# Kernel optimization log

Measured on AMD Instinct MI355X. Metric: run time of the kernel, lower is better.

The kernel has to match this reference:

```python
import jax, jax.numpy as jnp
import numpy as np

L, D, H, F, V, S, B = 6, 1024, 16, 4096, 32000, 1024, 2
HD = D // H  # head_dim = 64


def _rope_tables():
    freqs = 1.0 / (10000.0 ** (np.arange(0, HD, 2, dtype=np.float32) / HD))
    ang = np.outer(np.arange(S, dtype=np.float32), freqs)
    ang = np.concatenate([ang, ang], axis=-1)  # angles.repeat(1, 2)
    return jnp.asarray(np.cos(ang)), jnp.asarray(np.sin(ang))


def _ln(x, g, b):
    m = jnp.mean(x, -1, keepdims=True)
    v = jnp.mean((x - m) ** 2, -1, keepdims=True)
    return (x - m) * jax.lax.rsqrt(v + 1e-5) * g + b


def _rot_half(x):
    h = x.shape[-1] // 2
    return jnp.concatenate([-x[..., h:], x[..., :h]], -1)


def _gate(sig, W1, b1, W2, b2):
    h = jax.nn.gelu(sig @ W1 + b1, approximate=False)
    return jax.nn.sigmoid(h @ W2 + b2)[:, None, :]  # (B,1,D)


def setup_inputs():
    key = jax.random.key(0)
    ks = iter(jax.random.split(key, 40))

    def nrm(shape, s=0.02):
        return jax.random.normal(next(ks), shape, jnp.float32) * s

    cos, sin = _rope_tables()
    return {
        "input_ids": jax.random.randint(next(ks), (B, S), 0, V, dtype=jnp.int32),
        "gate_signals": jax.random.uniform(next(ks), (B, 3), jnp.float32),
        "tok_emb": nrm((V, D)),
        "rope_cos": cos, "rope_sin": sin,
        "Wq": nrm((L, D, D)), "bq": jnp.zeros((L, D)),
        "Wk": nrm((L, D, D)), "bk": jnp.zeros((L, D)),
        "Wv": nrm((L, D, D)), "bv": jnp.zeros((L, D)),
        "Wo": nrm((L, D, D)), "bo": jnp.zeros((L, D)),
        "ln1_g": jnp.ones((L, D)), "ln1_b": jnp.zeros((L, D)),
        "ln2_g": jnp.ones((L, D)), "ln2_b": jnp.zeros((L, D)),
        "W1": nrm((L, D, F)), "b1": jnp.zeros((L, F)),
        "W2": nrm((L, F, D)), "b2": jnp.zeros((L, D)),
        "ag_W1": nrm((L, 3, 32)), "ag_b1": jnp.zeros((L, 32)),
        "ag_W2": nrm((L, 32, D)), "ag_b2": jnp.full((L, D), 2.0, jnp.float32),
        "fg_W1": nrm((L, 3, 32)), "fg_b1": jnp.zeros((L, 32)),
        "fg_W2": nrm((L, 32, D)), "fg_b2": jnp.full((L, D), 2.0, jnp.float32),
        "lnf_g": jnp.ones((D,)), "lnf_b": jnp.zeros((D,)),
        "Wout": nrm((D, V)), "bout": jnp.zeros((V,)),
    }


def _forward(input_ids, gate_signals, tok_emb, rope_cos, rope_sin,
             Wq, bq, Wk, bk, Wv, bv, Wo, bo,
             ln1_g, ln1_b, ln2_g, ln2_b, W1, b1, W2, b2,
             ag_W1, ag_b1, ag_W2, ag_b2, fg_W1, fg_b1, fg_W2, fg_b2,
             lnf_g, lnf_b, Wout, bout):
    x = tok_emb[input_ids]  # (B,S,D)
    cos = rope_cos[None, :, None, :]  # broadcast over batch, heads
    sin = rope_sin[None, :, None, :]
    causal = jnp.triu(jnp.ones((S, S), bool), 1)
    scale = 1.0 / np.sqrt(HD).astype(np.float32)
    for i in range(L):
        n = _ln(x, ln1_g[i], ln1_b[i])
        q = (n @ Wq[i] + bq[i]).reshape(B, S, H, HD)
        k = (n @ Wk[i] + bk[i]).reshape(B, S, H, HD)
        v = (n @ Wv[i] + bv[i]).reshape(B, S, H, HD)
        q = q * cos + _rot_half(q) * sin
        k = k * cos + _rot_half(k) * sin
        scores = jnp.einsum("bqhd,bkhd->bhqk", q, k) * scale
        scores = jnp.where(causal[None, None], -jnp.inf, scores)
        attn = jax.nn.softmax(scores, axis=-1)
        ao = jnp.einsum("bhqk,bkhd->bqhd", attn, v).reshape(B, S, D)
        ao = (ao @ Wo[i] + bo[i]) * _gate(gate_signals, ag_W1[i], ag_b1[i], ag_W2[i], ag_b2[i])
        x = x + ao
        n = _ln(x, ln2_g[i], ln2_b[i])
        f = jax.nn.gelu(n @ W1[i] + b1[i], approximate=False) @ W2[i] + b2[i]
        f = f * _gate(gate_signals, fg_W1[i], fg_b1[i], fg_W2[i], fg_b2[i])
        x = x + f
    x = _ln(x, lnf_g, lnf_b)
    return x @ Wout + bout  # logits (B,S,V)


def reference(input_ids, gate_signals, tok_emb, rope_cos, rope_sin,
              Wq, bq, Wk, bk, Wv, bv, Wo, bo,
              ln1_g, ln1_b, ln2_g, ln2_b, W1, b1, W2, b2,
              ag_W1, ag_b1, ag_W2, ag_b2, fg_W1, fg_b1, fg_W2, fg_b2,
              lnf_g, lnf_b, Wout, bout):
    return _forward(input_ids, gate_signals, tok_emb, rope_cos, rope_sin,
                    Wq, bq, Wk, bk, Wv, bv, Wo, bo,
                    ln1_g, ln1_b, ln2_g, ln2_b, W1, b1, W2, b2,
                    ag_W1, ag_b1, ag_W2, ag_b2, fg_W1, fg_b1, fg_W2, fg_b2,
                    lnf_g, lnf_b, Wout, bout)
```

## Files before the change

kernel.cpp:

```cpp
#include <hip/hip_runtime.h>


typedef __attribute__((ext_vector_type(8))) short short8;
typedef __attribute__((ext_vector_type(4))) float f32x4;

__device__ inline unsigned short f2bf(float f) {
  unsigned u = __builtin_bit_cast(unsigned, f);
  u += 0x7fffu + ((u >> 16) & 1u);
  return (unsigned short)(u >> 16);
}

__device__ inline void gload_lds16(const unsigned short* g, unsigned short* l) {
  __builtin_amdgcn_global_load_lds(
      (const __attribute__((address_space(1))) void*)g,
      (__attribute__((address_space(3))) void*)l, 16, 0, 0);
}

__global__ __launch_bounds__(256) void transpose_k(
    const float* __restrict__ src, unsigned short* __restrict__ dst,
    int K, int N, size_t srcStride, size_t dstStride) {
  __shared__ __align__(16) float tile[32 * 33];
  src += (size_t)blockIdx.z * srcStride;
  dst += (size_t)blockIdx.z * dstStride;
  const int k0 = blockIdx.y * 32, n0 = blockIdx.x * 32;
  const int t = threadIdx.x;
  {
    int k = t >> 3, n4 = (t & 7) << 2;
    float4 v = *(const float4*)&src[(size_t)(k0 + k) * N + n0 + n4];
    tile[k * 33 + n4 + 0] = v.x; tile[k * 33 + n4 + 1] = v.y;
    tile[k * 33 + n4 + 2] = v.z; tile[k * 33 + n4 + 3] = v.w;
  }
  __syncthreads();
  {
    int n = t >> 3, k4 = (t & 7) << 2;
    ushort4 o;
    o.x = f2bf(tile[(k4 + 0) * 33 + n]);
    o.y = f2bf(tile[(k4 + 1) * 33 + n]);
    o.z = f2bf(tile[(k4 + 2) * 33 + n]);
    o.w = f2bf(tile[(k4 + 3) * 33 + n]);
    *(ushort4*)&dst[(size_t)(n0 + n) * K + k0 + k4] = o;
  }
}

__global__ __launch_bounds__(256) void embed_k(
    const int* __restrict__ ids, const float* __restrict__ emb,
    float* __restrict__ x) {
  const int m = blockIdx.x, t = threadIdx.x;
  const int id = ids[m];
  ((float4*)(x + (size_t)m * 1024))[t] = ((const float4*)(emb + (size_t)id * 1024))[t];
}

__global__ __launch_bounds__(256) void gates_k(
    const float* __restrict__ sig,
    const float* __restrict__ aW1, const float* __restrict__ ab1,
    const float* __restrict__ aW2, const float* __restrict__ ab2,
    const float* __restrict__ fW1, const float* __restrict__ fb1,
    const float* __restrict__ fW2, const float* __restrict__ fb2,
    float* __restrict__ gout) {
  const int b = blockIdx.x, l = blockIdx.y, w = blockIdx.z;
  const float* W1 = (w ? fW1 : aW1) + l * 96;
  const float* B1 = (w ? fb1 : ab1) + l * 32;
  const float* W2 = (w ? fW2 : aW2) + (size_t)l * 32 * 1024;
  const float* B2 = (w ? fb2 : ab2) + l * 1024;
  __shared__ float h[32];
  const int t = threadIdx.x;
  if (t < 32) {
    float a = sig[b * 3] * W1[t] + sig[b * 3 + 1] * W1[32 + t] + sig[b * 3 + 2] * W1[64 + t] + B1[t];
    h[t] = 0.5f * a * (1.0f + erff(a * 0.70710678118654752f));
  }
  __syncthreads();
  #pragma unroll
  for (int i = 0; i < 4; i++) {
    int d = t + i * 256;
    float a = B2[d];
    #pragma unroll
    for (int j = 0; j < 32; j++) a += h[j] * W2[j * 1024 + d];
    gout[(((size_t)w * 6 + l) * 2 + b) * 1024 + d] = 1.0f / (1.0f + expf(-a));
  }
}

__global__ __launch_bounds__(256) void ln_k(
    const float* __restrict__ x, const float* __restrict__ gw,
    const float* __restrict__ bw, unsigned short* __restrict__ out) {
  const int row = blockIdx.x, t = threadIdx.x;
  const float4 v = ((const float4*)(x + (size_t)row * 1024))[t];
  float s  = v.x + v.y + v.z + v.w;
  float s2 = v.x * v.x + v.y * v.y + v.z * v.z + v.w * v.w;
  #pragma unroll
  for (int m_ = 1; m_ < 64; m_ <<= 1) {
    s  += __shfl_xor(s, m_, 64);
    s2 += __shfl_xor(s2, m_, 64);
  }
  __shared__ float red[8];
  const int wv = t >> 6;
  if ((t & 63) == 0) { red[wv] = s; red[4 + wv] = s2; }
  __syncthreads();
  s  = red[0] + red[1] + red[2] + red[3];
  s2 = red[4] + red[5] + red[6] + red[7];
  const float mean = s * (1.0f / 1024.0f);
  const float var  = s2 * (1.0f / 1024.0f) - mean * mean;
  const float rstd = rsqrtf(var + 1e-5f);
  const float4 gv = ((const float4*)gw)[t];
  const float4 bv = ((const float4*)bw)[t];
  ushort4 o;
  o.x = f2bf((v.x - mean) * rstd * gv.x + bv.x);
  o.y = f2bf((v.y - mean) * rstd * gv.y + bv.y);
  o.z = f2bf((v.z - mean) * rstd * gv.z + bv.z);
  o.w = f2bf((v.w - mean) * rstd * gv.w + bv.w);
  ((ushort4*)(out + (size_t)row * 1024))[t] = o;
}

struct GArgs {
  const unsigned short *A, *Bt0, *Bt1, *Bt2;
  const float *bias0, *bias1, *bias2;
  unsigned short *ob0, *ob1, *ob2;
  float* xio;
  const float *gate, *ropec, *ropes;
  int M, N, K, epi;
};

template <int MT>
__global__ __launch_bounds__(256) void gemm_bt(GArgs g) {
  constexpr int BM = MT * 32;
  __shared__ __align__(16) unsigned short As[BM * 64];
  __shared__ __align__(16) unsigned short Bs[128 * 64];
  const int z = blockIdx.z;
  const unsigned short* A  = g.A;
  const unsigned short* Bt = (z == 0) ? g.Bt0 : (z == 1 ? g.Bt1 : g.Bt2);
  unsigned short* obf      = (z == 0) ? g.ob0 : (z == 1 ? g.ob1 : g.ob2);
  const float* bias        = (z == 0) ? g.bias0 : (z == 1 ? g.bias1 : g.bias2);
  const int m0 = blockIdx.y * BM, n0 = blockIdx.x * 128;
  const int t = threadIdx.x;
  const int wave = t >> 6, lane = t & 63, l16 = lane & 15, quad = lane >> 4;
  const int wm = wave >> 1, wn = wave & 1;
  const int K_ = g.K;

  const int srow = lane >> 3;
  const int scol = (lane & 7) ^ srow;

  const f32x4 vzero = {0.0f, 0.0f, 0.0f, 0.0f};
  f32x4 acc[MT][4];
  #pragma unroll
  for (int i = 0; i < MT; i++)
    #pragma unroll
    for (int j = 0; j < 4; j++) acc[i][j] = vzero;

  for (int k0 = 0; k0 < K_; k0 += 64) {
    __syncthreads();
    #pragma unroll
    for (int i = 0; i < MT; i++) {
      const int r0 = (wave * MT + i) * 8;
      gload_lds16(&A[(size_t)(m0 + r0 + srow) * K_ + k0 + scol * 8], &As[r0 * 64]);
    }
    #pragma unroll
    for (int i = 0; i < 4; i++) {
      const int r0 = (wave * 4 + i) * 8;
      gload_lds16(&Bt[(size_t)(n0 + r0 + srow) * K_ + k0 + scol * 8], &Bs[r0 * 64]);
    }
    __syncthreads();
    #pragma unroll
    for (int kk = 0; kk < 2; kk++) {
      short8 af[MT], bfr[4];
      #pragma unroll
      for (int mt = 0; mt < MT; mt++) {
        const int ar = wm * (MT * 16) + mt * 16 + l16;
        af[mt] = *(const short8*)&As[ar * 64 + (((kk * 4 + quad) ^ (ar & 7)) << 3)];
      }
      #pragma unroll
      for (int nt = 0; nt < 4; nt++) {
        const int br = wn * 64 + nt * 16 + l16;
        bfr[nt] = *(const short8*)&Bs[br * 64 + (((kk * 4 + quad) ^ (br & 7)) << 3)];
      }
      #pragma unroll
      for (int mt = 0; mt < MT; mt++)
        #pragma unroll
        for (int nt = 0; nt < 4; nt++)
          acc[mt][nt] = __builtin_amdgcn_mfma_f32_16x16x32_bf16(af[mt], bfr[nt], acc[mt][nt], 0, 0, 0);
    }
  }

  const int mbase = m0 + wm * (MT * 16) + quad * 4;
  const int nb = n0 + wn * 64 + l16;
  const size_t Nsz = (size_t)g.N;
  float bv4[4];
  #pragma unroll
  for (int nt = 0; nt < 4; nt++) bv4[nt] = bias[nb + nt * 16];

  if (g.epi == 1 && z < 2) {
    #pragma unroll
    for (int mt = 0; mt < MT; mt++) {
      float vv[4][4];
      #pragma unroll
      for (int nt = 0; nt < 4; nt++)
        #pragma unroll
        for (int r = 0; r < 4; r++) vv[nt][r] = acc[mt][nt][r] + bv4[nt];
      #pragma unroll
      for (int nt = 0; nt < 4; nt++) {
        const int d = (nb + nt * 16) & 63;
        #pragma unroll
        for (int r = 0; r < 4; r++) {
          const int m = mbase + mt * 16 + r;
          const int s = m & 1023;
          const float c = g.ropec[s * 64 + d], sn = g.ropes[s * 64 + d];
          const float rot = (nt < 2) ? -vv[nt + 2][r] : vv[nt - 2][r];
          obf[(size_t)m * Nsz + nb + nt * 16] = f2bf(vv[nt][r] * c + rot * sn);
        }
      }
    }
  } else if (g.epi <= 1) {
    #pragma unroll
    for (int mt = 0; mt < MT; mt++)
      #pragma unroll
      for (int nt = 0; nt < 4; nt++)
        #pragma unroll
        for (int r = 0; r < 4; r++)
          obf[(size_t)(mbase + mt * 16 + r) * Nsz + nb + nt * 16] = f2bf(acc[mt][nt][r] + bv4[nt]);
  } else if (g.epi == 2) {
    const int bb = m0 >> 10;
    float gt[4];
    #pragma unroll
    for (int nt = 0; nt < 4; nt++) gt[nt] = g.gate[bb * 1024 + nb + nt * 16];
    #pragma unroll
    for (int mt = 0; mt < MT; mt++)
      #pragma unroll
      for (int nt = 0; nt < 4; nt++)
        #pragma unroll
        for (int r = 0; r < 4; r++) {
          const size_t idx = (size_t)(mbase + mt * 16 + r) * Nsz + nb + nt * 16;
          g.xio[idx] += (acc[mt][nt][r] + bv4[nt]) * gt[nt];
        }
  } else if (g.epi == 3) {
    #pragma unroll
    for (int mt = 0; mt < MT; mt++)
      #pragma unroll
      for (int nt = 0; nt < 4; nt++)
        #pragma unroll
        for (int r = 0; r < 4; r++) {
          float vg = acc[mt][nt][r] + bv4[nt];
          vg = 0.5f * vg * (1.0f + erff(vg * 0.70710678118654752f));
          obf[(size_t)(mbase + mt * 16 + r) * Nsz + nb + nt * 16] = f2bf(vg);
        }
  } else {
    #pragma unroll
    for (int mt = 0; mt < MT; mt++)
      #pragma unroll
      for (int nt = 0; nt < 4; nt++)
        #pragma unroll
        for (int r = 0; r < 4; r++)
          g.xio[(size_t)(mbase + mt * 16 + r) * Nsz + nb + nt * 16] = acc[mt][nt][r] + bv4[nt];
  }
}

__global__ __launch_bounds__(64) void attn_k(
    const unsigned short* __restrict__ q, const unsigned short* __restrict__ k,
    const unsigned short* __restrict__ v, unsigned short* __restrict__ o) {
  __shared__ __align__(16) unsigned short Pl[32 * 72];
  __shared__ __align__(16) unsigned short Vt[64 * 72];
  const int lane = threadIdx.x, l16 = lane & 15, quad = lane >> 4;
  const int bh = blockIdx.y, b = bh >> 4, h = bh & 15;
  const int q0 = blockIdx.x * 32;
  const size_t base = (size_t)b * 1024 * 1024 + h * 64;
  const unsigned short* qh = q + base;
  const unsigned short* kh = k + base;
  const unsigned short* vh = v + base;
  unsigned short* oh = o + base;

  const f32x4 vzero = {0.0f, 0.0f, 0.0f, 0.0f};
  short8 qf[2][2];
  #pragma unroll
  for (int mt = 0; mt < 2; mt++)
    #pragma unroll
    for (int kt = 0; kt < 2; kt++)
      qf[mt][kt] = *(const short8*)&qh[(size_t)(q0 + mt * 16 + l16) * 1024 + kt * 32 + quad * 8];

  f32x4 oacc[2][4];
  float mrun[2][4], lrun[2][4];
  #pragma unroll
  for (int mt = 0; mt < 2; mt++) {
    #pragma unroll
    for (int jt = 0; jt < 4; jt++) oacc[mt][jt] = vzero;
    #pragma unroll
    for (int r = 0; r < 4; r++) { mrun[mt][r] = -1e30f; lrun[mt][r] = 0.0f; }
  }

  const int tmax = (q0 + 31) >> 6;
  for (int tt = 0; tt <= tmax; tt++) {
    const int s0 = tt * 64;
    short8 kf[4][2];
    #pragma unroll
    for (int st = 0; st < 4; st++)
      #pragma unroll
      for (int kt = 0; kt < 2; kt++)
        kf[st][kt] = *(const short8*)&kh[(size_t)(s0 + st * 16 + l16) * 1024 + kt * 32 + quad * 8];

    __syncthreads();
    {
      const int p = lane & 31, c0 = lane >> 5;
      #pragma unroll
      for (int i = 0; i < 4; i++) {
        const int d0 = (c0 + i * 2) * 8;
        uint4 va = *(const uint4*)&vh[(size_t)(s0 + 2 * p) * 1024 + d0];
        uint4 vb = *(const uint4*)&vh[(size_t)(s0 + 2 * p + 1) * 1024 + d0];
        const unsigned short* pa = (const unsigned short*)&va;
        const unsigned short* pb = (const unsigned short*)&vb;
        #pragma unroll
        for (int j = 0; j < 8; j++)
          *(unsigned*)&Vt[(d0 + j) * 72 + 2 * p] =
              (unsigned)pa[j] | ((unsigned)pb[j] << 16);
      }
    }

    f32x4 sacc[2][4];
    #pragma unroll
    for (int mt = 0; mt < 2; mt++)
      #pragma unroll
      for (int st = 0; st < 4; st++) sacc[mt][st] = vzero;
    #pragma unroll
    for (int mt = 0; mt < 2; mt++)
      #pragma unroll
      for (int st = 0; st < 4; st++)
        #pragma unroll
        for (int kt = 0; kt < 2; kt++)
          sacc[mt][st] = __builtin_amdgcn_mfma_f32_16x16x32_bf16(qf[mt][kt], kf[st][kt], sacc[mt][st], 0, 0, 0);

    float sv[2][4][4];
    #pragma unroll
    for (int mt = 0; mt < 2; mt++)
      #pragma unroll
      for (int st = 0; st < 4; st++)
        #pragma unroll
        for (int r = 0; r < 4; r++) {
          float x = sacc[mt][st][r] * 0.125f;
          if (tt == tmax) {
            const int qi = q0 + mt * 16 + quad * 4 + r;
            const int si = s0 + st * 16 + l16;
            if (si > qi) x = -1e30f;
          }
          sv[mt][st][r] = x;
        }

    float alpha[2][4];
    #pragma unroll
    for (int mt = 0; mt < 2; mt++)
      #pragma unroll
      for (int r = 0; r < 4; r++) {
        float rm = fmaxf(fmaxf(sv[mt][0][r], sv[mt][1][r]), fmaxf(sv[mt][2][r], sv[mt][3][r]));
        rm = fmaxf(rm, __shfl_xor(rm, 1, 64));
        rm = fmaxf(rm, __shfl_xor(rm, 2, 64));
        rm = fmaxf(rm, __shfl_xor(rm, 4, 64));
        rm = fmaxf(rm, __shfl_xor(rm, 8, 64));
        const float mn = fmaxf(mrun[mt][r], rm);
        alpha[mt][r] = __expf(mrun[mt][r] - mn);
        mrun[mt][r] = mn;
      }

    float psum[2][4] = {};
    #pragma unroll
    for (int mt = 0; mt < 2; mt++)
      #pragma unroll
      for (int st = 0; st < 4; st++)
        #pragma unroll
        for (int r = 0; r < 4; r++) {
          const float p_ = __expf(sv[mt][st][r] - mrun[mt][r]);
          psum[mt][r] += p_;
          Pl[(mt * 16 + quad * 4 + r) * 72 + st * 16 + l16] = f2bf(p_);
        }
    #pragma unroll
    for (int mt = 0; mt < 2; mt++)
      #pragma unroll
      for (int r = 0; r < 4; r++) {
        float ps = psum[mt][r];
        ps += __shfl_xor(ps, 1, 64);
        ps += __shfl_xor(ps, 2, 64);
        ps += __shfl_xor(ps, 4, 64);
        ps += __shfl_xor(ps, 8, 64);
        lrun[mt][r] = lrun[mt][r] * alpha[mt][r] + ps;
      }
    #pragma unroll
    for (int mt = 0; mt < 2; mt++)
      #pragma unroll
      for (int jt = 0; jt < 4; jt++)
        #pragma unroll
        for (int r = 0; r < 4; r++) oacc[mt][jt][r] *= alpha[mt][r];

    __syncthreads();
    short8 pf[2][2], vf[4][2];
    #pragma unroll
    for (int mt = 0; mt < 2; mt++)
      #pragma unroll
      for (int kt = 0; kt < 2; kt++)
        pf[mt][kt] = *(const short8*)&Pl[(mt * 16 + l16) * 72 + kt * 32 + quad * 8];
    #pragma unroll
    for (int jt = 0; jt < 4; jt++)
      #pragma unroll
      for (int kt = 0; kt < 2; kt++)
        vf[jt][kt] = *(const short8*)&Vt[(jt * 16 + l16) * 72 + kt * 32 + quad * 8];
    #pragma unroll
    for (int mt = 0; mt < 2; mt++)
      #pragma unroll
      for (int jt = 0; jt < 4; jt++)
        #pragma unroll
        for (int kt = 0; kt < 2; kt++)
          oacc[mt][jt] = __builtin_amdgcn_mfma_f32_16x16x32_bf16(pf[mt][kt], vf[jt][kt], oacc[mt][jt], 0, 0, 0);
  }

  #pragma unroll
  for (int mt = 0; mt < 2; mt++)
    #pragma unroll
    for (int r = 0; r < 4; r++) {
      const float inv = 1.0f / lrun[mt][r];
      const int qrow = q0 + mt * 16 + quad * 4 + r;
      #pragma unroll
      for (int jt = 0; jt < 4; jt++)
        oh[(size_t)qrow * 1024 + jt * 16 + l16] = f2bf(oacc[mt][jt][r] * inv);
    }
}

extern "C" void kernel_launch(void* const* d_in, const int* in_sizes, int n_in,
                              void* d_out, int out_size, void* d_ws, size_t ws_size,
                              hipStream_t stream) {
  const int*   ids   = (const int*)d_in[0];
  const float* sig   = (const float*)d_in[1];
  const float* temb  = (const float*)d_in[2];
  const float* ropec = (const float*)d_in[3];
  const float* ropes = (const float*)d_in[4];
  const float* Wq = (const float*)d_in[5],  *bq = (const float*)d_in[6];
  const float* Wk = (const float*)d_in[7],  *bk = (const float*)d_in[8];
  const float* Wv = (const float*)d_in[9],  *bv = (const float*)d_in[10];
  const float* Wo = (const float*)d_in[11], *bo = (const float*)d_in[12];
  const float* ln1g = (const float*)d_in[13], *ln1b = (const float*)d_in[14];
  const float* ln2g = (const float*)d_in[15], *ln2b = (const float*)d_in[16];
  const float* W1 = (const float*)d_in[17], *b1 = (const float*)d_in[18];
  const float* W2 = (const float*)d_in[19], *b2 = (const float*)d_in[20];
  const float* agW1 = (const float*)d_in[21], *agb1 = (const float*)d_in[22];
  const float* agW2 = (const float*)d_in[23], *agb2 = (const float*)d_in[24];
  const float* fgW1 = (const float*)d_in[25], *fgb1 = (const float*)d_in[26];
  const float* fgW2 = (const float*)d_in[27], *fgb2 = (const float*)d_in[28];
  const float* lnfg = (const float*)d_in[29], *lnfb = (const float*)d_in[30];
  const float* Wout = (const float*)d_in[31], *bout = (const float*)d_in[32];

  const size_t DD = 1024 * 1024;
  uintptr_t w = (uintptr_t)d_ws;
  auto take = [&](size_t bytes) -> uintptr_t {
    uintptr_t p = w; w += (bytes + 255) & ~(size_t)255; return p;
  };
  unsigned short* wt_qkv = (unsigned short*)take((size_t)6 * 3 * DD * 2);
  unsigned short* wt_o   = (unsigned short*)take((size_t)6 * DD * 2);
  unsigned short* wt_1   = (unsigned short*)take((size_t)6 * 4096 * 1024 * 2);
  unsigned short* wt_2   = (unsigned short*)take((size_t)6 * 1024 * 4096 * 2);
  unsigned short* wt_out = (unsigned short*)take((size_t)32000 * 1024 * 2);
  float*          xbuf   = (float*)take((size_t)2048 * 1024 * 4);
  unsigned short* nbuf   = (unsigned short*)take((size_t)2048 * 1024 * 2);
  unsigned short* qbuf   = (unsigned short*)take((size_t)3 * 2048 * 1024 * 2);
  unsigned short* kbuf   = qbuf + (size_t)2048 * 1024;
  unsigned short* vbuf   = kbuf + (size_t)2048 * 1024;
  unsigned short* aobuf  = (unsigned short*)take((size_t)2048 * 1024 * 2);
  unsigned short* hbuf   = (unsigned short*)take((size_t)2048 * 4096 * 2);
  float*          gbuf   = (float*)take((size_t)2 * 6 * 2 * 1024 * 4);

  transpose_k<<<dim3(32, 32, 6),  256, 0, stream>>>(Wq, wt_qkv + 0 * DD, 1024, 1024, DD, 3 * DD);
  transpose_k<<<dim3(32, 32, 6),  256, 0, stream>>>(Wk, wt_qkv + 1 * DD, 1024, 1024, DD, 3 * DD);
  transpose_k<<<dim3(32, 32, 6),  256, 0, stream>>>(Wv, wt_qkv + 2 * DD, 1024, 1024, DD, 3 * DD);
  transpose_k<<<dim3(32, 32, 6),  256, 0, stream>>>(Wo, wt_o, 1024, 1024, DD, DD);
  transpose_k<<<dim3(128, 32, 6), 256, 0, stream>>>(W1, wt_1, 1024, 4096, (size_t)4096 * 1024, (size_t)4096 * 1024);
  transpose_k<<<dim3(32, 128, 6), 256, 0, stream>>>(W2, wt_2, 4096, 1024, (size_t)4096 * 1024, (size_t)4096 * 1024);
  transpose_k<<<dim3(1000, 32, 1), 256, 0, stream>>>(Wout, wt_out, 1024, 32000, 0, 0);

  gates_k<<<dim3(2, 6, 2), 256, 0, stream>>>(sig, agW1, agb1, agW2, agb2, fgW1, fgb1, fgW2, fgb2, gbuf);
  embed_k<<<dim3(2048), 256, 0, stream>>>(ids, temb, xbuf);

  for (int l = 0; l < 6; l++) {
    ln_k<<<2048, 256, 0, stream>>>(xbuf, ln1g + l * 1024, ln1b + l * 1024, nbuf);

    GArgs a{};
    a.A = nbuf;
    a.Bt0 = wt_qkv + (size_t)(l * 3 + 0) * DD;
    a.Bt1 = wt_qkv + (size_t)(l * 3 + 1) * DD;
    a.Bt2 = wt_qkv + (size_t)(l * 3 + 2) * DD;
    a.bias0 = bq + l * 1024; a.bias1 = bk + l * 1024; a.bias2 = bv + l * 1024;
    a.ob0 = qbuf; a.ob1 = kbuf; a.ob2 = vbuf;
    a.ropec = ropec; a.ropes = ropes;
    a.M = 2048; a.N = 1024; a.K = 1024; a.epi = 1;
    gemm_bt<4><<<dim3(8, 16, 3), 256, 0, stream>>>(a);

    attn_k<<<dim3(32, 32), 64, 0, stream>>>(qbuf, kbuf, vbuf, aobuf);

    GArgs c{};
    c.A = aobuf; c.Bt0 = wt_o + (size_t)l * DD; c.bias0 = bo + l * 1024;
    c.xio = xbuf; c.gate = gbuf + (size_t)l * 2 * 1024;
    c.M = 2048; c.N = 1024; c.K = 1024; c.epi = 2;
    gemm_bt<2><<<dim3(8, 32, 1), 256, 0, stream>>>(c);

    ln_k<<<2048, 256, 0, stream>>>(xbuf, ln2g + l * 1024, ln2b + l * 1024, nbuf);

    GArgs f1{};
    f1.A = nbuf; f1.Bt0 = wt_1 + (size_t)l * 4096 * 1024; f1.bias0 = b1 + l * 4096;
    f1.ob0 = hbuf; f1.M = 2048; f1.N = 4096; f1.K = 1024; f1.epi = 3;
    gemm_bt<4><<<dim3(32, 16, 1), 256, 0, stream>>>(f1);

    GArgs f2{};
    f2.A = hbuf; f2.Bt0 = wt_2 + (size_t)l * 1024 * 4096; f2.bias0 = b2 + l * 1024;
    f2.xio = xbuf; f2.gate = gbuf + (size_t)(6 + l) * 2 * 1024;
    f2.M = 2048; f2.N = 1024; f2.K = 4096; f2.epi = 2;
    gemm_bt<2><<<dim3(8, 32, 1), 256, 0, stream>>>(f2);
  }

  ln_k<<<2048, 256, 0, stream>>>(xbuf, lnfg, lnfb, nbuf);

  GArgs lo{};
  lo.A = nbuf; lo.Bt0 = wt_out; lo.bias0 = bout;
  lo.xio = (float*)d_out;
  lo.M = 2048; lo.N = 32000; lo.K = 1024; lo.epi = 5;
  gemm_bt<4><<<dim3(250, 16, 1), 256, 0, stream>>>(lo);
}
```

Baseline: 2.235 ms.

## Remap GEMM blocks across XCDs and split attention across two waves

Measured after the change: 2.259 ms. Within noise of the previous version (+1.1%).

```diff
diff --git a/kernel.cpp b/kernel.cpp
--- a/kernel.cpp
+++ b/kernel.cpp
@@ -129,7 +129,17 @@
   const unsigned short* Bt = (z == 0) ? g.Bt0 : (z == 1 ? g.Bt1 : g.Bt2);
   unsigned short* obf      = (z == 0) ? g.ob0 : (z == 1 ? g.ob1 : g.ob2);
   const float* bias        = (z == 0) ? g.bias0 : (z == 1 ? g.bias1 : g.bias2);
-  const int m0 = blockIdx.y * BM, n0 = blockIdx.x * 128;
+
+  const int nwg  = gridDim.x * gridDim.y;
+  const int hwid = blockIdx.y * gridDim.x + blockIdx.x;
+  const int xcd = hwid & 7, j8 = hwid >> 3;
+  const int q8 = nwg >> 3, r8 = nwg & 7;
+  const int logical =
+      (xcd < r8 ? xcd * (q8 + 1) : r8 * (q8 + 1) + (xcd - r8) * q8) + j8;
+  const int mIdx = logical % gridDim.y;
+  const int nIdx = logical / gridDim.y;
+  const int m0 = mIdx * BM, n0 = nIdx * 128;
+
   const int t = threadIdx.x;
   const int wave = t >> 6, lane = t & 63, l16 = lane & 15, quad = lane >> 4;
   const int wm = wave >> 1, wn = wave & 1;
@@ -251,37 +261,35 @@
   }
 }
 
-__global__ __launch_bounds__(64) void attn_k(
+__global__ __launch_bounds__(128) void attn_k(
     const unsigned short* __restrict__ q, const unsigned short* __restrict__ k,
     const unsigned short* __restrict__ v, unsigned short* __restrict__ o) {
-  __shared__ __align__(16) unsigned short Pl[32 * 72];
+  __shared__ __align__(16) unsigned short Pl[2 * 16 * 72];
   __shared__ __align__(16) unsigned short Vt[64 * 72];
-  const int lane = threadIdx.x, l16 = lane & 15, quad = lane >> 4;
+  const int t = threadIdx.x;
+  const int wave = t >> 6, lane = t & 63, l16 = lane & 15, quad = lane >> 4;
   const int bh = blockIdx.y, b = bh >> 4, h = bh & 15;
   const int q0 = blockIdx.x * 32;
+  const int qw = q0 + wave * 16;
   const size_t base = (size_t)b * 1024 * 1024 + h * 64;
   const unsigned short* qh = q + base;
   const unsigned short* kh = k + base;
   const unsigned short* vh = v + base;
   unsigned short* oh = o + base;
+  unsigned short* Pw = Pl + wave * 16 * 72;
 
   const f32x4 vzero = {0.0f, 0.0f, 0.0f, 0.0f};
-  short8 qf[2][2];
-  #pragma unroll
-  for (int mt = 0; mt < 2; mt++)
-    #pragma unroll
-    for (int kt = 0; kt < 2; kt++)
-      qf[mt][kt] = *(const short8*)&qh[(size_t)(q0 + mt * 16 + l16) * 1024 + kt * 32 + quad * 8];
-
-  f32x4 oacc[2][4];
-  float mrun[2][4], lrun[2][4];
-  #pragma unroll
-  for (int mt = 0; mt < 2; mt++) {
-    #pragma unroll
-    for (int jt = 0; jt < 4; jt++) oacc[mt][jt] = vzero;
-    #pragma unroll
-    for (int r = 0; r < 4; r++) { mrun[mt][r] = -1e30f; lrun[mt][r] = 0.0f; }
-  }
+  short8 qf[2];
+  #pragma unroll
+  for (int kt = 0; kt < 2; kt++)
+    qf[kt] = *(const short8*)&qh[(size_t)(qw + l16) * 1024 + kt * 32 + quad * 8];
+
+  f32x4 oacc[4];
+  float mrun[4], lrun[4];
+  #pragma unroll
+  for (int jt = 0; jt < 4; jt++) oacc[jt] = vzero;
+  #pragma unroll
+  for (int r = 0; r < 4; r++) { mrun[r] = -1e30f; lrun[r] = 0.0f; }
 
   const int tmax = (q0 + 31) >> 6;
   for (int tt = 0; tt <= tmax; tt++) {
@@ -295,125 +303,105 @@
 
     __syncthreads();
     {
-      const int p = lane & 31, c0 = lane >> 5;
-      #pragma unroll
-      for (int i = 0; i < 4; i++) {
-        const int d0 = (c0 + i * 2) * 8;
+      const int p = t & 31, c0 = t >> 5;
+      #pragma unroll
+      for (int i = 0; i < 2; i++) {
+        const int d0 = (c0 + i * 4) * 8;
         uint4 va = *(const uint4*)&vh[(size_t)(s0 + 2 * p) * 1024 + d0];
         uint4 vb = *(const uint4*)&vh[(size_t)(s0 + 2 * p + 1) * 1024 + d0];
         const unsigned short* pa = (const unsigned short*)&va;
         const unsigned short* pb = (const unsigned short*)&vb;
         #pragma unroll
-        for (int j = 0; j < 8; j++)
-          *(unsigned*)&Vt[(d0 + j) * 72 + 2 * p] =
-              (unsigned)pa[j] | ((unsigned)pb[j] << 16);
+        for (int jj = 0; jj < 8; jj++)
+          *(unsigned*)&Vt[(d0 + jj) * 72 + 2 * p] =
+              (unsigned)pa[jj] | ((unsigned)pb[jj] << 16);
       }
     }
 
-    f32x4 sacc[2][4];
-    #pragma unroll
-    for (int mt = 0; mt < 2; mt++)
-      #pragma unroll
-      for (int st = 0; st < 4; st++) sacc[mt][st] = vzero;
-    #pragma unroll
-    for (int mt = 0; mt < 2; mt++)
-      #pragma unroll
-      for (int st = 0; st < 4; st++)
-        #pragma unroll
-        for (int kt = 0; kt < 2; kt++)
-          sacc[mt][st] = __builtin_amdgcn_mfma_f32_16x16x32_bf16(qf[mt][kt], kf[st][kt], sacc[mt][st], 0, 0, 0);
-
-    float sv[2][4][4];
-    #pragma unroll
-    for (int mt = 0; mt < 2; mt++)
-      #pragma unroll
-      for (int st = 0; st < 4; st++)
-        #pragma unroll
-        for (int r = 0; r < 4; r++) {
-          float x = sacc[mt][st][r] * 0.125f;
-          if (tt == tmax) {
-            const int qi = q0 + mt * 16 + quad * 4 + r;
-            const int si = s0 + st * 16 + l16;
-            if (si > qi) x = -1e30f;
-          }
-          sv[mt][st][r] = x;
+    f32x4 sacc[4];
+    #pragma unroll
+    for (int st = 0; st < 4; st++) sacc[st] = vzero;
+    #pragma unroll
+    for (int st = 0; st < 4; st++)
+      #pragma unroll
+      for (int kt = 0; kt < 2; kt++)
+        sacc[st] = __builtin_amdgcn_mfma_f32_16x16x32_bf16(qf[kt], kf[st][kt], sacc[st], 0, 0, 0);
+
+    float sv[4][4];
+    #pragma unroll
+    for (int st = 0; st < 4; st++)
+      #pragma unroll
+      for (int r = 0; r < 4; r++) {
+        float x = sacc[st][r] * 0.125f;
+        if (tt == tmax) {
+          const int qi = qw + quad * 4 + r;
+          const int si = s0 + st * 16 + l16;
+          if (si > qi) x = -1e30f;
         }
-
-    float alpha[2][4];
-    #pragma unroll
-    for (int mt = 0; mt < 2; mt++)
+        sv[st][r] = x;
+      }
+
+    float alpha[4];
+    #pragma unroll
+    for (int r = 0; r < 4; r++) {
+      float rm = fmaxf(fmaxf(sv[0][r], sv[1][r]), fmaxf(sv[2][r], sv[3][r]));
+      rm = fmaxf(rm, __shfl_xor(rm, 1, 64));
+      rm = fmaxf(rm, __shfl_xor(rm, 2, 64));
+      rm = fmaxf(rm, __shfl_xor(rm, 4, 64));
+      rm = fmaxf(rm, __shfl_xor(rm, 8, 64));
+      const float mn = fmaxf(mrun[r], rm);
+      alpha[r] = __expf(mrun[r] - mn);
+      mrun[r] = mn;
+    }
+
+    float psum[4] = {};
+    #pragma unroll
+    for (int st = 0; st < 4; st++)
       #pragma unroll
       for (int r = 0; r < 4; r++) {
-        float rm = fmaxf(fmaxf(sv[mt][0][r], sv[mt][1][r]), fmaxf(sv[mt][2][r], sv[mt][3][r]));
-        rm = fmaxf(rm, __shfl_xor(rm, 1, 64));
-        rm = fmaxf(rm, __shfl_xor(rm, 2, 64));
-        rm = fmaxf(rm, __shfl_xor(rm, 4, 64));
-        rm = fmaxf(rm, __shfl_xor(rm, 8, 64));
-        const float mn = fmaxf(mrun[mt][r], rm);
-        alpha[mt][r] = __expf(mrun[mt][r] - mn);
-        mrun[mt][r] = mn;
+        const float p_ = __expf(sv[st][r] - mrun[r]);
+        psum[r] += p_;
+        Pw[(quad * 4 + r) * 72 + st * 16 + l16] = f2bf(p_);
       }
-
-    float psum[2][4] = {};
-    #pragma unroll
-    for (int mt = 0; mt < 2; mt++)
-      #pragma unroll
-      for (int st = 0; st < 4; st++)
-        #pragma unroll
-        for (int r = 0; r < 4; r++) {
-          const float p_ = __expf(sv[mt][st][r] - mrun[mt][r]);
-          psum[mt][r] += p_;
-          Pl[(mt * 16 + quad * 4 + r) * 72 + st * 16 + l16] = f2bf(p_);
-        }
-    #pragma unroll
-    for (int mt = 0; mt < 2; mt++)
-      #pragma unroll
-      for (int r = 0; r < 4; r++) {
-        float ps = psum[mt][r];
-        ps += __shfl_xor(ps, 1, 64);
-        ps += __shfl_xor(ps, 2, 64);
-        ps += __shfl_xor(ps, 4, 64);
-        ps += __shfl_xor(ps, 8, 64);
-        lrun[mt][r] = lrun[mt][r] * alpha[mt][r] + ps;
-      }
-    #pragma unroll
-    for (int mt = 0; mt < 2; mt++)
-      #pragma unroll
-      for (int jt = 0; jt < 4; jt++)
-        #pragma unroll
-        for (int r = 0; r < 4; r++) oacc[mt][jt][r] *= alpha[mt][r];
+    #pragma unroll
+    for (int r = 0; r < 4; r++) {
+      float ps = psum[r];
+      ps += __shfl_xor(ps, 1, 64);
+      ps += __shfl_xor(ps, 2, 64);
+      ps += __shfl_xor(ps, 4, 64);
+      ps += __shfl_xor(ps, 8, 64);
+      lrun[r] = lrun[r] * alpha[r] + ps;
+    }
+    #pragma unroll
+    for (int jt = 0; jt < 4; jt++)
+      #pragma unroll
+      for (int r = 0; r < 4; r++) oacc[jt][r] *= alpha[r];
 
     __syncthreads();
-    short8 pf[2][2], vf[4][2];
-    #pragma unroll
-    for (int mt = 0; mt < 2; mt++)
-      #pragma unroll
-      for (int kt = 0; kt < 2; kt++)
-        pf[mt][kt] = *(const short8*)&Pl[(mt * 16 + l16) * 72 + kt * 32 + quad * 8];
+    short8 pf[2], vf[4][2];
+    #pragma unroll
+    for (int kt = 0; kt < 2; kt++)
+      pf[kt] = *(const short8*)&Pw[l16 * 72 + kt * 32 + quad * 8];
     #pragma unroll
     for (int jt = 0; jt < 4; jt++)
       #pragma unroll
       for (int kt = 0; kt < 2; kt++)
         vf[jt][kt] = *(const short8*)&Vt[(jt * 16 + l16) * 72 + kt * 32 + quad * 8];
     #pragma unroll
-    for (int mt = 0; mt < 2; mt++)
-      #pragma unroll
-      for (int jt = 0; jt < 4; jt++)
-        #pragma unroll
-        for (int kt = 0; kt < 2; kt++)
-          oacc[mt][jt] = __builtin_amdgcn_mfma_f32_16x16x32_bf16(pf[mt][kt], vf[jt][kt], oacc[mt][jt], 0, 0, 0);
-  }
-
-  #pragma unroll
-  for (int mt = 0; mt < 2; mt++)
-    #pragma unroll
-    for (int r = 0; r < 4; r++) {
-      const float inv = 1.0f / lrun[mt][r];
-      const int qrow = q0 + mt * 16 + quad * 4 + r;
-      #pragma unroll
-      for (int jt = 0; jt < 4; jt++)
-        oh[(size_t)qrow * 1024 + jt * 16 + l16] = f2bf(oacc[mt][jt][r] * inv);
-    }
+    for (int jt = 0; jt < 4; jt++)
+      #pragma unroll
+      for (int kt = 0; kt < 2; kt++)
+        oacc[jt] = __builtin_amdgcn_mfma_f32_16x16x32_bf16(pf[kt], vf[jt][kt], oacc[jt], 0, 0, 0);
+  }
+
+  #pragma unroll
+  for (int r = 0; r < 4; r++) {
+    const float inv = 1.0f / lrun[r];
+    const int qrow = qw + quad * 4 + r;
+    #pragma unroll
+    for (int jt = 0; jt < 4; jt++)
+      oh[(size_t)qrow * 1024 + jt * 16 + l16] = f2bf(oacc[jt][r] * inv);
+  }
 }
 
 extern "C" void kernel_launch(void* const* d_in, const int* in_sizes, int n_in,
@@ -483,7 +471,7 @@
     a.M = 2048; a.N = 1024; a.K = 1024; a.epi = 1;
     gemm_bt<4><<<dim3(8, 16, 3), 256, 0, stream>>>(a);
 
-    attn_k<<<dim3(32, 32), 64, 0, stream>>>(qbuf, kbuf, vbuf, aobuf);
+    attn_k<<<dim3(32, 32), 128, 0, stream>>>(qbuf, kbuf, vbuf, aobuf);
 
     GArgs c{};
     c.A = aobuf; c.Bt0 = wt_o + (size_t)l * DD; c.bias0 = bo + l * 1024;
```
